# Optimization experiments

Hardware: AMD Instinct MI355X
Metric: run time of the kernel (lower is better)

Reference implementation:

```python
import jax, jax.numpy as jnp
import numpy as np


def setup_inputs() -> dict:
    key = jax.random.key(0)
    ks = jax.random.split(key, 8)
    Bsz, L, D, N, R = 2, 2048, 2048, 16, 128
    x = jax.random.normal(ks[0], (Bsz, L, D), jnp.float32)
    delta = jax.random.normal(ks[1], (Bsz, L, R), jnp.float32)
    B_in = jax.random.normal(ks[2], (Bsz, L, N), jnp.float32)
    C_in = jax.random.normal(ks[3], (Bsz, L, N), jnp.float32)
    # dt_proj params (scaled small so softplus(dt) stays in a sane range)
    W_dt = jax.random.normal(ks[4], (D, R), jnp.float32) * 0.02
    b_dt = jax.random.normal(ks[5], (D,), jnp.float32) * 0.02
    # A_log = log(uniform(0,1)) as in the torch init -> A = -exp(A_log) in (-1, 0)
    A_log = jnp.log(jax.random.uniform(ks[6], (D, N), jnp.float32, 1e-4, 1.0))
    D_param = jnp.ones((D,), jnp.float32)
    return {"x": x, "delta": delta, "B_in": B_in, "C_in": C_in,
            "W_dt": W_dt, "b_dt": b_dt, "A_log": A_log, "D_param": D_param}


def reference(x, delta, B_in, C_in, W_dt, b_dt, A_log, D_param):
    # dt = softplus(dt_proj(delta))  -> (B, L, D)
    dt = jax.nn.softplus(jnp.einsum('blr,dr->bld', delta, W_dt) + b_dt)
    A = -jnp.exp(A_log)                                  # (D, N)
    decay = jnp.exp(jnp.einsum('bld,dn->bldn', dt, A))   # exp(dt*A): (B, L, D, N)
    u = jnp.einsum('bld,bln->bldn', dt * x, B_in)        # dt*B*x input term
    # move length to leading axis for scan
    aT = jnp.moveaxis(decay, 1, 0)   # (L, B, D, N)
    uT = jnp.moveaxis(u, 1, 0)       # (L, B, D, N)
    cT = jnp.moveaxis(C_in, 1, 0)    # (L, B, N)

    h0 = jnp.zeros((x.shape[0], x.shape[2], A.shape[1]), x.dtype)  # (B, D, N)

    def step(h, inp):
        a, uu, c = inp
        h = a * h + uu                              # selective state update
        y = jnp.einsum('bdn,bn->bd', h, c)          # readout
        return h, y

    _, ys = jax.lax.scan(step, h0, (aT, uT, cT))    # ys: (L, B, D)
    return jnp.moveaxis(ys, 0, 1) + x * D_param
```

## Files before the change

kernel.cpp:

```cpp
#include <hip/hip_runtime.h>
#include <hip/hip_bf16.h>
#include <math.h>

namespace {

constexpr int BSZ = 2, LEN = 2048, DIM = 2048, NST = 16, RNK = 128;
constexpr int NC = 64, CHUNK = LEN / NC;
constexpr int KS = 3 * RNK;
constexpr float LOG2E = 1.4426950408889634f;
constexpr float LN2 = 0.6931471805599453f;

using bf16x8 = __attribute__((ext_vector_type(8))) short;
using f32x4  = __attribute__((ext_vector_type(4))) float;

__device__ __forceinline__ float fast_exp2(float x) {
#if __has_builtin(__builtin_amdgcn_exp2f)
  return __builtin_amdgcn_exp2f(x);
#else
  return exp2f(x);
#endif
}

__device__ __forceinline__ unsigned short bf16_rne(float x) {
  __hip_bfloat16 h = __float2bfloat16(x);
  return *(unsigned short*)&h;
}
__device__ __forceinline__ float bf16_tof(unsigned short u) {
  __hip_bfloat16 h = *(__hip_bfloat16*)&u;
  return __bfloat162float(h);
}

__global__ __launch_bounds__(256)
void split_bf16(const float* __restrict__ delta, const float* __restrict__ W,
                unsigned short* __restrict__ Ad, unsigned short* __restrict__ Bd) {
  int t = blockIdx.x * 256 + threadIdx.x;
  const int NA = BSZ * LEN * RNK;
  if (t < NA) {
    int row = t >> 7, k = t & (RNK - 1);
    float x = delta[t];
    unsigned short hi = bf16_rne(x);
    unsigned short lo = bf16_rne(x - bf16_tof(hi));
    unsigned short* p = Ad + (size_t)row * KS;
    p[k] = hi; p[RNK + k] = lo; p[2 * RNK + k] = hi;
  } else {
    t -= NA;
    int row = t >> 7, k = t & (RNK - 1);
    float x = W[t];
    unsigned short hi = bf16_rne(x);
    unsigned short lo = bf16_rne(x - bf16_tof(hi));
    unsigned short* p = Bd + (size_t)row * KS;
    p[k] = hi; p[RNK + k] = hi; p[2 * RNK + k] = lo;
  }
}

__global__ __launch_bounds__(256)
void dt_mfma(const unsigned short* __restrict__ Ad, const unsigned short* __restrict__ Bd,
             const float* __restrict__ bias, float* __restrict__ dtout) {
  const int lane = threadIdx.x & 63, wid = threadIdx.x >> 6;
  const int wm = wid >> 1, wn = wid & 1;
  const int bm = blockIdx.x & 31, bn = blockIdx.x >> 5;
  const int r = lane & 15, kg = lane >> 4;

  const unsigned short* arow = Ad + (size_t)(bm * 128 + wm * 64 + r) * KS + kg * 8;
  const unsigned short* brow = Bd + (size_t)(bn * 128 + wn * 64 + r) * KS + kg * 8;

  f32x4 acc[4][4] = {};
#pragma unroll
  for (int ks = 0; ks < KS / 32; ++ks) {
    bf16x8 af[4], bf[4];
#pragma unroll
    for (int m = 0; m < 4; ++m)
      af[m] = *(const bf16x8*)(arow + (size_t)m * 16 * KS + ks * 32);
#pragma unroll
    for (int n = 0; n < 4; ++n)
      bf[n] = *(const bf16x8*)(brow + (size_t)n * 16 * KS + ks * 32);
#pragma unroll
    for (int m = 0; m < 4; ++m)
#pragma unroll
      for (int n = 0; n < 4; ++n)
        acc[m][n] = __builtin_amdgcn_mfma_f32_16x16x32_bf16(af[m], bf[n], acc[m][n], 0, 0, 0);
  }

#pragma unroll
  for (int n = 0; n < 4; ++n) {
    const int col = bn * 128 + wn * 64 + n * 16 + r;
    const float bs = bias[col];
#pragma unroll
    for (int m = 0; m < 4; ++m) {
      const int row0 = bm * 128 + wm * 64 + m * 16 + kg * 4;
#pragma unroll
      for (int j = 0; j < 4; ++j) {
        float z = acc[m][n][j] + bs;
        float sp = fmaxf(z, 0.f) + LN2 * __log2f(1.0f + fast_exp2(-fabsf(z) * LOG2E));
        dtout[(size_t)(row0 + j) * DIM + col] = sp;
      }
    }
  }
}

__global__ __launch_bounds__(256)
void scan1_ns(const float* __restrict__ dtw, const float* __restrict__ x,
              const float* __restrict__ Bin, const float* __restrict__ Alog,
              float* __restrict__ Sout, float* __restrict__ sdtout) {
  __shared__ float dt_l[CHUNK][32];
  __shared__ float x_l[CHUNK][32];
  __shared__ float B_l[CHUNK][NST];
  const int tid = threadIdx.x;
  const int bz = blockIdx.x;
  const int dgrp = bz & 63;
  const int c = (bz >> 6) & (NC - 1);
  const int b = bz >> 12;
  const int l0 = c * CHUNK;
  const int nt = tid & 7, dl = tid >> 3;
  const int d = dgrp * 32 + dl;
  const int n0 = nt * 2;

  const float* dtp = dtw + ((size_t)b * LEN + l0) * DIM + dgrp * 32;
  const float* xp  = x   + ((size_t)b * LEN + l0) * DIM + dgrp * 32;
#pragma unroll
  for (int j = 0; j < 4; ++j) {
    int idx = tid + j * 256, row = idx >> 5, col = idx & 31;
    dt_l[row][col] = dtp[(size_t)row * DIM + col];
    x_l[row][col]  = xp[(size_t)row * DIM + col];
  }
#pragma unroll
  for (int j = 0; j < 2; ++j) {
    int idx = tid + j * 256, row = idx >> 4, nn = idx & 15;
    B_l[row][nn] = Bin[((size_t)b * LEN + l0 + row) * NST + nn];
  }
  float2 al = *(const float2*)&Alog[(size_t)d * NST + n0];
  const float a20 = -expf(al.x) * LOG2E;
  const float a21 = -expf(al.y) * LOG2E;
  __syncthreads();

  float h0 = 0.f, h1 = 0.f, sdt = 0.f;
#pragma unroll
  for (int i = 0; i < CHUNK; ++i) {
    float dt = dt_l[i][dl];
    float dtx = dt * x_l[i][dl];
    sdt += dt;
    float e0 = fast_exp2(dt * a20);
    float e1 = fast_exp2(dt * a21);
    h0 = fmaf(e0, h0, dtx * B_l[i][n0]);
    h1 = fmaf(e1, h1, dtx * B_l[i][n0 + 1]);
  }
  const size_t ob = ((size_t)(b * NC + c) * DIM + d) * NST + n0;
  float2 hv; hv.x = h0; hv.y = h1;
  *(float2*)&Sout[ob] = hv;
  if (nt == 0) sdtout[(size_t)(b * NC + c) * DIM + d] = sdt;
}

__global__ __launch_bounds__(256)
void chunk_combine(const float* __restrict__ sdt, float* __restrict__ S,
                   const float* __restrict__ Alog) {
  const int t = blockIdx.x * 256 + threadIdx.x;
  const int n = t & (NST - 1);
  const int d = (t >> 4) & (DIM - 1);
  const int b = t >> 15;
  const float a2 = -expf(Alog[(size_t)d * NST + n]) * LOG2E;

  float pfS[8], pfD[8];
#pragma unroll
  for (int c = 0; c < 8; ++c) {
    const size_t idx = ((size_t)(b * NC + c) * DIM + d) * NST + n;
    pfS[c] = S[idx];
    pfD[c] = sdt[(size_t)(b * NC + c) * DIM + d];
  }
  float cur = 0.f;
#pragma unroll
  for (int c = 0; c < NC; ++c) {
    const size_t idx = ((size_t)(b * NC + c) * DIM + d) * NST + n;
    float s = pfS[c & 7];
    float sd = pfD[c & 7];
    S[idx] = cur;
    if (c + 8 < NC) {
      const size_t idx8 = ((size_t)(b * NC + c + 8) * DIM + d) * NST + n;
      pfS[c & 7] = S[idx8];
      pfD[c & 7] = sdt[(size_t)(b * NC + c + 8) * DIM + d];
    }
    cur = fmaf(fast_exp2(sd * a2), cur, s);
  }
}

__global__ __launch_bounds__(256)
void scan2_ns(const float* __restrict__ dtw, const float* __restrict__ x,
              const float* __restrict__ Bin, const float* __restrict__ Cin,
              const float* __restrict__ Alog, const float* __restrict__ Dpar,
              const float* __restrict__ Hin, float* __restrict__ out) {
  __shared__ float dt_l[CHUNK][32];
  __shared__ float x_l[CHUNK][32];
  __shared__ float B_l[CHUNK][NST];
  __shared__ float C_l[CHUNK][NST];
  const int tid = threadIdx.x;
  const int bz = blockIdx.x;
  const int dgrp = bz & 63;
  const int c = (bz >> 6) & (NC - 1);
  const int b = bz >> 12;
  const int l0 = c * CHUNK;
  const int nt = tid & 7, dl = tid >> 3;
  const int d = dgrp * 32 + dl;
  const int n0 = nt * 2;

  const float* dtp = dtw + ((size_t)b * LEN + l0) * DIM + dgrp * 32;
  const float* xp  = x   + ((size_t)b * LEN + l0) * DIM + dgrp * 32;
#pragma unroll
  for (int j = 0; j < 4; ++j) {
    int idx = tid + j * 256, row = idx >> 5, col = idx & 31;
    dt_l[row][col] = dtp[(size_t)row * DIM + col];
    x_l[row][col]  = xp[(size_t)row * DIM + col];
  }
#pragma unroll
  for (int j = 0; j < 2; ++j) {
    int idx = tid + j * 256, row = idx >> 4, nn = idx & 15;
    B_l[row][nn] = Bin[((size_t)b * LEN + l0 + row) * NST + nn];
    C_l[row][nn] = Cin[((size_t)b * LEN + l0 + row) * NST + nn];
  }
  float2 al = *(const float2*)&Alog[(size_t)d * NST + n0];
  const float a20 = -expf(al.x) * LOG2E;
  const float a21 = -expf(al.y) * LOG2E;
  const float dpar = Dpar[d];

  const size_t ob = ((size_t)(b * NC + c) * DIM + d) * NST + n0;
  float2 hv = *(const float2*)&Hin[ob];
  float h0 = hv.x, h1 = hv.y;
  __syncthreads();

  float* op = out + ((size_t)b * LEN + l0) * DIM + d;

#pragma unroll
  for (int i = 0; i < CHUNK; ++i) {
    float dt = dt_l[i][dl];
    float xv = x_l[i][dl];
    float dtx = dt * xv;
    float e0 = fast_exp2(dt * a20);
    float e1 = fast_exp2(dt * a21);
    h0 = fmaf(e0, h0, dtx * B_l[i][n0]);
    h1 = fmaf(e1, h1, dtx * B_l[i][n0 + 1]);
    float yp = h0 * C_l[i][n0];
    yp = fmaf(h1, C_l[i][n0 + 1], yp);
    yp += __shfl_xor(yp, 1, 8);
    yp += __shfl_xor(yp, 2, 8);
    yp += __shfl_xor(yp, 4, 8);
    if (nt == 0) op[(size_t)i * DIM] = fmaf(xv, dpar, yp);
  }
}

}

extern "C" void kernel_launch(void* const* d_in, const int* in_sizes, int n_in,
                              void* d_out, int out_size, void* d_ws, size_t ws_size,
                              hipStream_t stream) {
  const float* x     = (const float*)d_in[0];
  const float* delta = (const float*)d_in[1];
  const float* Bin   = (const float*)d_in[2];
  const float* Cin   = (const float*)d_in[3];
  const float* Wdt   = (const float*)d_in[4];
  const float* bdt   = (const float*)d_in[5];
  const float* Alog  = (const float*)d_in[6];
  const float* Dpar  = (const float*)d_in[7];
  float* out = (float*)d_out;

  char* ws = (char*)d_ws;
  size_t off = 0;
  float* dtw = (float*)(ws + off); off += (size_t)BSZ * LEN * DIM * 4;
  float* S   = (float*)(ws + off); off += (size_t)BSZ * NC * DIM * NST * 4;
  float* sdt = (float*)(ws + off); off += (size_t)BSZ * NC * DIM * 4;
  unsigned short* Ad = (unsigned short*)(ws + off); off += (size_t)BSZ * LEN * KS * 2;
  unsigned short* Bd = (unsigned short*)(ws + off); off += (size_t)DIM * KS * 2;

  split_bf16<<<(BSZ * LEN * RNK + DIM * RNK) / 256, 256, 0, stream>>>(delta, Wdt, Ad, Bd);
  dt_mfma<<<(BSZ * LEN / 128) * (DIM / 128), 256, 0, stream>>>(Ad, Bd, bdt, dtw);
  scan1_ns<<<BSZ * NC * (DIM / 32), 256, 0, stream>>>(dtw, x, Bin, Alog, S, sdt);
  chunk_combine<<<BSZ * DIM * NST / 256, 256, 0, stream>>>(sdt, S, Alog);
  scan2_ns<<<BSZ * NC * (DIM / 32), 256, 0, stream>>>(dtw, x, Bin, Cin, Alog, Dpar, S, out);
}
```

Measured before the change: 200.1 us.

## Fuse chunked scan passes into a single persistent sequential scan kernel

Replaces the three-kernel chunked scan (per-chunk partial states, chunk combine, rescan with readout) with one kernel per (batch, 16-channel group) that walks the whole sequence once. It double-buffers 32-step tiles in LDS and prefetches the next tile into registers. The readout over the 16 states now uses DPP lane adds instead of shuffles. This removes the second read of dt and x, the state workspace traffic and two launches. In exchange, each block runs a long serial loop with only one tile of prefetch and two barriers per tile, so memory latency may be poorly hidden with just one block per CU.

```diff
diff --git a/kernel.cpp b/kernel.cpp
--- a/kernel.cpp
+++ b/kernel.cpp
@@ -28,6 +28,12 @@
 __device__ __forceinline__ float bf16_tof(unsigned short u) {
   __hip_bfloat16 h = *(__hip_bfloat16*)&u;
   return __bfloat162float(h);
+}
+
+template <int CTRL>
+__device__ __forceinline__ float dpp_add_f(float v) {
+  int p = __builtin_amdgcn_update_dpp(0, __float_as_int(v), CTRL, 0xF, 0xF, true);
+  return v + __int_as_float(p);
 }
 
 __global__ __launch_bounds__(256)
@@ -98,150 +104,90 @@
   }
 }
 
-__global__ __launch_bounds__(256)
-void scan1_ns(const float* __restrict__ dtw, const float* __restrict__ x,
-              const float* __restrict__ Bin, const float* __restrict__ Alog,
-              float* __restrict__ Sout, float* __restrict__ sdtout) {
-  __shared__ float dt_l[CHUNK][32];
-  __shared__ float x_l[CHUNK][32];
-  __shared__ float B_l[CHUNK][NST];
+__global__ __launch_bounds__(256, 1)
+void scan_persist(const float* __restrict__ dtw, const float* __restrict__ x,
+                  const float* __restrict__ Bin, const float* __restrict__ Cin,
+                  const float* __restrict__ Alog, const float* __restrict__ Dpar,
+                  float* __restrict__ out) {
+  __shared__ __align__(16) float dt_t[2][16][36];
+  __shared__ __align__(16) float x_t [2][16][36];
+  __shared__ __align__(16) float B_t [2][16][36];
+  __shared__ __align__(16) float C_t [2][16][36];
   const int tid = threadIdx.x;
-  const int bz = blockIdx.x;
-  const int dgrp = bz & 63;
-  const int c = (bz >> 6) & (NC - 1);
-  const int b = bz >> 12;
-  const int l0 = c * CHUNK;
-  const int nt = tid & 7, dl = tid >> 3;
-  const int d = dgrp * 32 + dl;
-  const int n0 = nt * 2;
-
-  const float* dtp = dtw + ((size_t)b * LEN + l0) * DIM + dgrp * 32;
-  const float* xp  = x   + ((size_t)b * LEN + l0) * DIM + dgrp * 32;
-#pragma unroll
-  for (int j = 0; j < 4; ++j) {
-    int idx = tid + j * 256, row = idx >> 5, col = idx & 31;
-    dt_l[row][col] = dtp[(size_t)row * DIM + col];
-    x_l[row][col]  = xp[(size_t)row * DIM + col];
-  }
-#pragma unroll
-  for (int j = 0; j < 2; ++j) {
-    int idx = tid + j * 256, row = idx >> 4, nn = idx & 15;
-    B_l[row][nn] = Bin[((size_t)b * LEN + l0 + row) * NST + nn];
-  }
-  float2 al = *(const float2*)&Alog[(size_t)d * NST + n0];
-  const float a20 = -expf(al.x) * LOG2E;
-  const float a21 = -expf(al.y) * LOG2E;
+  const int dgrp = blockIdx.x & 127;
+  const int b = blockIdx.x >> 7;
+  const int dl = tid >> 4, nt = tid & 15;
+  const int d = dgrp * 16 + dl;
+
+  const float a2 = -expf(Alog[(size_t)d * NST + nt]) * LOG2E;
+  const float dpar = Dpar[d];
+
+  const int srow = tid >> 3;
+  const int scol = (tid & 7) * 2;
+  const float* dtp = dtw + (size_t)b * LEN * DIM + dgrp * 16;
+  const float* xp  = x   + (size_t)b * LEN * DIM + dgrp * 16;
+  const float* Bp  = Bin + (size_t)b * LEN * NST;
+  const float* Cp  = Cin + (size_t)b * LEN * NST;
+
+  {
+    float2 vdt = *(const float2*)&dtp[(size_t)srow * DIM + scol];
+    float2 vx  = *(const float2*)&xp [(size_t)srow * DIM + scol];
+    float2 vB  = *(const float2*)&Bp [(size_t)srow * NST + scol];
+    float2 vC  = *(const float2*)&Cp [(size_t)srow * NST + scol];
+    dt_t[0][scol][srow] = vdt.x; dt_t[0][scol + 1][srow] = vdt.y;
+    x_t [0][scol][srow] = vx.x;  x_t [0][scol + 1][srow] = vx.y;
+    B_t [0][scol][srow] = vB.x;  B_t [0][scol + 1][srow] = vB.y;
+    C_t [0][scol][srow] = vC.x;  C_t [0][scol + 1][srow] = vC.y;
+  }
   __syncthreads();
 
-  float h0 = 0.f, h1 = 0.f, sdt = 0.f;
-#pragma unroll
-  for (int i = 0; i < CHUNK; ++i) {
-    float dt = dt_l[i][dl];
-    float dtx = dt * x_l[i][dl];
-    sdt += dt;
-    float e0 = fast_exp2(dt * a20);
-    float e1 = fast_exp2(dt * a21);
-    h0 = fmaf(e0, h0, dtx * B_l[i][n0]);
-    h1 = fmaf(e1, h1, dtx * B_l[i][n0 + 1]);
-  }
-  const size_t ob = ((size_t)(b * NC + c) * DIM + d) * NST + n0;
-  float2 hv; hv.x = h0; hv.y = h1;
-  *(float2*)&Sout[ob] = hv;
-  if (nt == 0) sdtout[(size_t)(b * NC + c) * DIM + d] = sdt;
-}
-
-__global__ __launch_bounds__(256)
-void chunk_combine(const float* __restrict__ sdt, float* __restrict__ S,
-                   const float* __restrict__ Alog) {
-  const int t = blockIdx.x * 256 + threadIdx.x;
-  const int n = t & (NST - 1);
-  const int d = (t >> 4) & (DIM - 1);
-  const int b = t >> 15;
-  const float a2 = -expf(Alog[(size_t)d * NST + n]) * LOG2E;
-
-  float pfS[8], pfD[8];
-#pragma unroll
-  for (int c = 0; c < 8; ++c) {
-    const size_t idx = ((size_t)(b * NC + c) * DIM + d) * NST + n;
-    pfS[c] = S[idx];
-    pfD[c] = sdt[(size_t)(b * NC + c) * DIM + d];
-  }
-  float cur = 0.f;
-#pragma unroll
+  float h = 0.f;
+  float* op = out + (size_t)b * LEN * DIM + d;
+
   for (int c = 0; c < NC; ++c) {
-    const size_t idx = ((size_t)(b * NC + c) * DIM + d) * NST + n;
-    float s = pfS[c & 7];
-    float sd = pfD[c & 7];
-    S[idx] = cur;
-    if (c + 8 < NC) {
-      const size_t idx8 = ((size_t)(b * NC + c + 8) * DIM + d) * NST + n;
-      pfS[c & 7] = S[idx8];
-      pfD[c & 7] = sdt[(size_t)(b * NC + c + 8) * DIM + d];
-    }
-    cur = fmaf(fast_exp2(sd * a2), cur, s);
-  }
-}
-
-__global__ __launch_bounds__(256)
-void scan2_ns(const float* __restrict__ dtw, const float* __restrict__ x,
-              const float* __restrict__ Bin, const float* __restrict__ Cin,
-              const float* __restrict__ Alog, const float* __restrict__ Dpar,
-              const float* __restrict__ Hin, float* __restrict__ out) {
-  __shared__ float dt_l[CHUNK][32];
-  __shared__ float x_l[CHUNK][32];
-  __shared__ float B_l[CHUNK][NST];
-  __shared__ float C_l[CHUNK][NST];
-  const int tid = threadIdx.x;
-  const int bz = blockIdx.x;
-  const int dgrp = bz & 63;
-  const int c = (bz >> 6) & (NC - 1);
-  const int b = bz >> 12;
-  const int l0 = c * CHUNK;
-  const int nt = tid & 7, dl = tid >> 3;
-  const int d = dgrp * 32 + dl;
-  const int n0 = nt * 2;
-
-  const float* dtp = dtw + ((size_t)b * LEN + l0) * DIM + dgrp * 32;
-  const float* xp  = x   + ((size_t)b * LEN + l0) * DIM + dgrp * 32;
-#pragma unroll
-  for (int j = 0; j < 4; ++j) {
-    int idx = tid + j * 256, row = idx >> 5, col = idx & 31;
-    dt_l[row][col] = dtp[(size_t)row * DIM + col];
-    x_l[row][col]  = xp[(size_t)row * DIM + col];
-  }
-#pragma unroll
-  for (int j = 0; j < 2; ++j) {
-    int idx = tid + j * 256, row = idx >> 4, nn = idx & 15;
-    B_l[row][nn] = Bin[((size_t)b * LEN + l0 + row) * NST + nn];
-    C_l[row][nn] = Cin[((size_t)b * LEN + l0 + row) * NST + nn];
-  }
-  float2 al = *(const float2*)&Alog[(size_t)d * NST + n0];
-  const float a20 = -expf(al.x) * LOG2E;
-  const float a21 = -expf(al.y) * LOG2E;
-  const float dpar = Dpar[d];
-
-  const size_t ob = ((size_t)(b * NC + c) * DIM + d) * NST + n0;
-  float2 hv = *(const float2*)&Hin[ob];
-  float h0 = hv.x, h1 = hv.y;
-  __syncthreads();
-
-  float* op = out + ((size_t)b * LEN + l0) * DIM + d;
-
-#pragma unroll
-  for (int i = 0; i < CHUNK; ++i) {
-    float dt = dt_l[i][dl];
-    float xv = x_l[i][dl];
-    float dtx = dt * xv;
-    float e0 = fast_exp2(dt * a20);
-    float e1 = fast_exp2(dt * a21);
-    h0 = fmaf(e0, h0, dtx * B_l[i][n0]);
-    h1 = fmaf(e1, h1, dtx * B_l[i][n0 + 1]);
-    float yp = h0 * C_l[i][n0];
-    yp = fmaf(h1, C_l[i][n0 + 1], yp);
-    yp += __shfl_xor(yp, 1, 8);
-    yp += __shfl_xor(yp, 2, 8);
-    yp += __shfl_xor(yp, 4, 8);
-    if (nt == 0) op[(size_t)i * DIM] = fmaf(xv, dpar, yp);
+    const int cur = c & 1, nxt = cur ^ 1;
+    const int l0 = c * CHUNK;
+    float2 ndt, nx, nB, nC;
+    if (c + 1 < NC) {
+      const size_t ro = (size_t)(l0 + CHUNK + srow);
+      ndt = *(const float2*)&dtp[ro * DIM + scol];
+      nx  = *(const float2*)&xp [ro * DIM + scol];
+      nB  = *(const float2*)&Bp [ro * NST + scol];
+      nC  = *(const float2*)&Cp [ro * NST + scol];
+    }
+    float ysv0 = 0.f, ysv1 = 0.f;
+#pragma unroll
+    for (int i4 = 0; i4 < CHUNK / 4; ++i4) {
+      const float4 dtv = *(const float4*)&dt_t[cur][dl][i4 * 4];
+      const float4 xv4 = *(const float4*)&x_t [cur][dl][i4 * 4];
+      const float4 Bv  = *(const float4*)&B_t [cur][nt][i4 * 4];
+      const float4 Cv  = *(const float4*)&C_t [cur][nt][i4 * 4];
+#pragma unroll
+      for (int ii = 0; ii < 4; ++ii) {
+        const int i = i4 * 4 + ii;
+        const float dt = (&dtv.x)[ii];
+        const float xv = (&xv4.x)[ii];
+        const float e  = fast_exp2(dt * a2);
+        h = fmaf(e, h, dt * xv * (&Bv.x)[ii]);
+        float y = h * (&Cv.x)[ii];
+        y = dpp_add_f<0xB1>(y);
+        y = dpp_add_f<0x4E>(y);
+        y = dpp_add_f<0x140>(y);
+        y = dpp_add_f<0x141>(y);
+        const float ov = fmaf(xv, dpar, y);
+        if ((i & 15) == nt) { if (i < 16) ysv0 = ov; else ysv1 = ov; }
+      }
+    }
+    op[(size_t)(l0 + nt) * DIM] = ysv0;
+    op[(size_t)(l0 + 16 + nt) * DIM] = ysv1;
+    if (c + 1 < NC) {
+      __syncthreads();
+      dt_t[nxt][scol][srow] = ndt.x; dt_t[nxt][scol + 1][srow] = ndt.y;
+      x_t [nxt][scol][srow] = nx.x;  x_t [nxt][scol + 1][srow] = nx.y;
+      B_t [nxt][scol][srow] = nB.x;  B_t [nxt][scol + 1][srow] = nB.y;
+      C_t [nxt][scol][srow] = nC.x;  C_t [nxt][scol + 1][srow] = nC.y;
+      __syncthreads();
+    }
   }
 }
 
@@ -263,14 +209,10 @@
   char* ws = (char*)d_ws;
   size_t off = 0;
   float* dtw = (float*)(ws + off); off += (size_t)BSZ * LEN * DIM * 4;
-  float* S   = (float*)(ws + off); off += (size_t)BSZ * NC * DIM * NST * 4;
-  float* sdt = (float*)(ws + off); off += (size_t)BSZ * NC * DIM * 4;
   unsigned short* Ad = (unsigned short*)(ws + off); off += (size_t)BSZ * LEN * KS * 2;
   unsigned short* Bd = (unsigned short*)(ws + off); off += (size_t)DIM * KS * 2;
 
   split_bf16<<<(BSZ * LEN * RNK + DIM * RNK) / 256, 256, 0, stream>>>(delta, Wdt, Ad, Bd);
   dt_mfma<<<(BSZ * LEN / 128) * (DIM / 128), 256, 0, stream>>>(Ad, Bd, bdt, dtw);
-  scan1_ns<<<BSZ * NC * (DIM / 32), 256, 0, stream>>>(dtw, x, Bin, Alog, S, sdt);
-  chunk_combine<<<BSZ * DIM * NST / 256, 256, 0, stream>>>(sdt, S, Alog);
-  scan2_ns<<<BSZ * NC * (DIM / 32), 256, 0, stream>>>(dtw, x, Bin, Cin, Alog, Dpar, S, out);
-}
+  scan_persist<<<BSZ * (DIM / 16), 256, 0, stream>>>(dtw, x, Bin, Cin, Alog, Dpar, out);
+}
```

Result: slower. 230.9 us (+15.4%).
